# Kernel tuning notes

Hardware: AMD Instinct MI355X
Metric: run time of the kernel (lower is better)

## Reference

```python
import jax, jax.numpy as jnp
import numpy as np

D_MODEL = 4096
D_LATENT = 512
NUM_HEADS = 32
HEAD_DIM = D_MODEL // NUM_HEADS  # 128
ROPE_THETA = 10000.0
BATCH, SEQ = 2, 2048


def _rotate_half(x):
    x1, x2 = jnp.split(x, 2, axis=-1)
    return jnp.concatenate([-x2, x1], axis=-1)


def _rope_cos_sin(positions, head_dim, theta, dtype):
    # positions: [B, S] -> cos/sin: [B, S, 1, head_dim]
    inv_freq = 1.0 / (theta ** (jnp.arange(0, head_dim, 2, dtype=jnp.float32) / head_dim))
    freqs = positions.astype(jnp.float32)[..., None] * inv_freq  # [B,S,hd/2]
    emb = jnp.concatenate([freqs, freqs], axis=-1)               # [B,S,hd]
    return jnp.cos(emb)[:, :, None, :].astype(dtype), jnp.sin(emb)[:, :, None, :].astype(dtype)


def setup_inputs() -> dict:
    key = jax.random.key(0)
    ks = jax.random.split(key, 6)
    s = 0.02
    return {
        "hidden_states": jax.random.normal(ks[0], (BATCH, SEQ, D_MODEL), jnp.float32),
        "Wq": jax.random.normal(ks[1], (D_MODEL, NUM_HEADS * HEAD_DIM), jnp.float32) * s,
        "Wc": jax.random.normal(ks[2], (D_MODEL, D_LATENT), jnp.float32) * s,
        "Wk": jax.random.normal(ks[3], (D_LATENT, NUM_HEADS * HEAD_DIM), jnp.float32) * s,
        "Wv": jax.random.normal(ks[4], (D_LATENT, NUM_HEADS * HEAD_DIM), jnp.float32) * s,
        "Wo": jax.random.normal(ks[5], (NUM_HEADS * HEAD_DIM, D_MODEL), jnp.float32) * s,
    }


def reference(hidden_states, Wq, Wc, Wk, Wv, Wo):
    B, S, _ = hidden_states.shape
    H, Dh = NUM_HEADS, HEAD_DIM

    q = (hidden_states @ Wq).reshape(B, S, H, Dh)
    kv_latent = hidden_states @ Wc                     # [B,S,d_latent]
    k = (kv_latent @ Wk).reshape(B, S, H, Dh)
    v = (kv_latent @ Wv).reshape(B, S, H, Dh)

    # RoPE: q uses positions [0..S), k uses positions [0..S) (no past cache)
    pos = jnp.broadcast_to(jnp.arange(S)[None, :], (B, S))
    cos, sin = _rope_cos_sin(pos, Dh, ROPE_THETA, q.dtype)
    q = q * cos + _rotate_half(q) * sin
    k = k * cos + _rotate_half(k) * sin

    # standard attention, no mask (faithful to attention_mask=None path)
    scale = 1.0 / np.sqrt(Dh)
    scores = jnp.einsum("bqhd,bkhd->bhqk", q, k) * scale
    probs = jax.nn.softmax(scores, axis=-1)
    attn = jnp.einsum("bhqk,bkhd->bqhd", probs, v)     # [B,S,H,Dh]

    out = attn.reshape(B, S, H * Dh) @ Wo
    return out
```

## Files before the change

### kernel.cpp

```cpp
#include <hip/hip_runtime.h>
#include <hip/hip_bf16.h>
#include <cstdint>
#include <cstddef>

#define D_MODEL 4096
#define D_LATENT 512
#define NUM_HEADS 32
#define HEAD_DIM 128
#define BATCH 2
#define SEQ 2048
#define ROWS (BATCH*SEQ)

typedef __attribute__((ext_vector_type(8))) short bf16x8;
typedef __attribute__((ext_vector_type(4))) float f32x4;
typedef __attribute__((ext_vector_type(16))) float f32x16;
typedef unsigned int uint;

static __device__ __forceinline__ unsigned short f2bf(float f){
  union { float f; uint32_t u; } v; v.f = f;
  uint32_t r = (v.u + 0x7fffu + ((v.u >> 16) & 1u)) >> 16;
  return (unsigned short)r;
}
static __device__ __forceinline__ float bf2f(unsigned short h){
  union { uint32_t u; float f; } v; v.u = ((uint32_t)h) << 16;
  return v.f;
}
static __device__ __forceinline__ uint cvtpk(float lo, float hi2){
  uint r;
  asm("v_cvt_pk_bf16_f32 %0, %1, %2" : "=v"(r) : "v"(lo), "v"(hi2));
  return r;
}
static __device__ __forceinline__ void gload16(const void* g, void* l){
  __builtin_amdgcn_global_load_lds(
      (const __attribute__((address_space(1))) void*)g,
      (__attribute__((address_space(3))) void*)l, 16, 0, 0);
}

__global__ __launch_bounds__(256) void f32_to_bf16(
    const float* __restrict__ in, unsigned short* __restrict__ out){
  const size_t i = ((size_t)blockIdx.x * 256 + threadIdx.x) * 8;
  const float4 lo = *(const float4*)(in + i);
  const float4 hi = *(const float4*)(in + i + 4);
  uint4 d; unsigned short* dp = (unsigned short*)&d;
  dp[0]=f2bf(lo.x); dp[1]=f2bf(lo.y); dp[2]=f2bf(lo.z); dp[3]=f2bf(lo.w);
  dp[4]=f2bf(hi.x); dp[5]=f2bf(hi.y); dp[6]=f2bf(hi.z); dp[7]=f2bf(hi.w);
  *(uint4*)(out + i) = d;
}

__global__ __launch_bounds__(256) void transpose_convert(
    const float* __restrict__ W, unsigned short* __restrict__ Wt, int K, int N){
  __shared__ float tile[64][65];
  const int k0 = blockIdx.x * 64, n0 = blockIdx.y * 64;
  const int t = threadIdx.x;
  #pragma unroll
  for (int j = 0; j < 16; ++j){
    const int idx = t + 256*j;
    const int r = idx >> 6, c = idx & 63;
    tile[r][c] = W[(size_t)(k0 + r) * N + n0 + c];
  }
  __syncthreads();
  #pragma unroll
  for (int j = 0; j < 16; ++j){
    const int idx = t + 256*j;
    const int r = idx >> 6, c = idx & 63;
    Wt[(size_t)(n0 + r) * K + k0 + c] = f2bf(tile[c][r]);
  }
}

__global__ __launch_bounds__(256) void v_transpose(
    const unsigned short* __restrict__ v, unsigned short* __restrict__ vt){
  __shared__ unsigned short tile[64][72];
  const int s0 = blockIdx.x * 64, d0 = blockIdx.y * 64, bh = blockIdx.z;
  const int b = bh >> 5, h = bh & 31;
  const int t = threadIdx.x;
  #pragma unroll
  for (int j = 0; j < 2; ++j){
    const int idx = t + 256*j;
    const int r = idx >> 3, ch = idx & 7;
    *(uint4*)&tile[r][ch*8] =
      *(const uint4*)&v[(size_t)(b*SEQ + s0 + r) * D_MODEL + h*128 + d0 + ch*8];
  }
  __syncthreads();
  #pragma unroll
  for (int j = 0; j < 16; ++j){
    const int idx = t + 256*j;
    const int r = idx >> 6, c = idx & 63;
    vt[((size_t)bh*128 + d0 + r) * SEQ + s0 + c] = tile[c][r];
  }
}

__global__ __launch_bounds__(256) void rope_table_kernel(float* __restrict__ ct,
                                                         float* __restrict__ st){
  const int i = blockIdx.x * 256 + threadIdx.x;
  if (i >= SEQ * 64) return;
  const int s = i >> 6, j = i & 63;
  const float inv = powf(10000.0f, -(float)j / 64.0f);
  const double a = (double)s * (double)inv;
  ct[i] = (float)cos(a);
  st[i] = (float)sin(a);
}

__global__ __launch_bounds__(256) void rope_apply(unsigned short* __restrict__ buf,
    const float* __restrict__ ct, const float* __restrict__ st, float scale){
  const int i = blockIdx.x * 256 + threadIdx.x;
  const int j = i & 63;
  const int tmp = i >> 6;
  const int h = tmp & 31;
  const int row = tmp >> 5;
  const int s = row & (SEQ - 1);
  const float c = ct[s*64 + j], sn = st[s*64 + j];
  const size_t base = (size_t)row * D_MODEL + (size_t)h * 128;
  const float x1 = bf2f(buf[base + j]);
  const float x2 = bf2f(buf[base + j + 64]);
  buf[base + j]      = f2bf((x1 * c - x2 * sn) * scale);
  buf[base + j + 64] = f2bf((x2 * c + x1 * sn) * scale);
}

template<bool OF32>
__global__ __launch_bounds__(256) void gemm_kernel(
    const unsigned short* __restrict__ A, const unsigned short* __restrict__ Bt,
    void* __restrict__ Cp, int M, int N, int K){
  __shared__ __align__(16) char As[128 * 128];
  __shared__ __align__(16) char Bs[128 * 128];
  const int t = threadIdx.x;
  const int m0 = blockIdx.y * 128, n0 = blockIdx.x * 128;
  const int l = t & 63, wid = t >> 6;
  const int wr = wid >> 1, wcn = wid & 1;
  const int lr = l & 15, lg = l >> 4;

  const int srow = l >> 3;
  const int gch  = (l & 7) ^ srow;
  const unsigned short* gA = A  + (size_t)(m0 + wid*32 + srow) * K + gch*8;
  const unsigned short* gB = Bt + (size_t)(n0 + wid*32 + srow) * K + gch*8;
  char* lA = As + wid*4096;
  char* lB = Bs + wid*4096;

  f32x4 acc[4][4];
  #pragma unroll
  for (int i = 0; i < 4; ++i)
    #pragma unroll
    for (int j = 0; j < 4; ++j)
      #pragma unroll
      for (int r = 0; r < 4; ++r) acc[i][j][r] = 0.0f;

  const int kTiles = K >> 6;
  for (int kt = 0; kt < kTiles; ++kt){
    const size_t ko = (size_t)kt << 6;
    #pragma unroll
    for (int i = 0; i < 4; ++i){
      gload16(gA + (size_t)i*8*K + ko, lA + i*1024);
      gload16(gB + (size_t)i*8*K + ko, lB + i*1024);
    }
    __syncthreads();
    #pragma unroll
    for (int kc = 0; kc < 2; ++kc){
      bf16x8 af[4], bfv[4];
      const int ch = kc*4 + lg;
      #pragma unroll
      for (int mb = 0; mb < 4; ++mb){
        const int row = wr*64 + mb*16 + lr;
        af[mb] = *(const bf16x8*)(As + row*128 + ((ch ^ (row & 7)) * 16));
      }
      #pragma unroll
      for (int nb = 0; nb < 4; ++nb){
        const int row = wcn*64 + nb*16 + lr;
        bfv[nb] = *(const bf16x8*)(Bs + row*128 + ((ch ^ (row & 7)) * 16));
      }
      #pragma unroll
      for (int mb = 0; mb < 4; ++mb)
        #pragma unroll
        for (int nb = 0; nb < 4; ++nb)
          acc[mb][nb] = __builtin_amdgcn_mfma_f32_16x16x32_bf16(af[mb], bfv[nb], acc[mb][nb], 0, 0, 0);
    }
    __syncthreads();
  }
  #pragma unroll
  for (int mb = 0; mb < 4; ++mb)
    #pragma unroll
    for (int nb = 0; nb < 4; ++nb)
      #pragma unroll
      for (int r = 0; r < 4; ++r){
        const int row = m0 + wr*64 + mb*16 + lg*4 + r;
        const int col = n0 + wcn*64 + nb*16 + lr;
        if constexpr (OF32) ((float*)Cp)[(size_t)row * N + col] = acc[mb][nb][r];
        else ((unsigned short*)Cp)[(size_t)row * N + col] = f2bf(acc[mb][nb][r]);
      }
}

template<int MH>
static __device__ __forceinline__ void rdAh(bf16x8 (&a_)[4][2], const char* buf,
                                            int wr, int lr, int lg){
  #pragma unroll
  for (int mm = 0; mm < 4; ++mm)
    #pragma unroll
    for (int kc = 0; kc < 2; ++kc){
      const int row = wr*128 + (MH*4 + mm)*16 + lr;
      const int ch = kc*4 + lg;
      a_[mm][kc] = *(const bf16x8*)(buf + row*128 + ((ch ^ (row & 7)) * 16));
    }
}
template<int NH>
static __device__ __forceinline__ void rdBh(bf16x8 (&b_)[2][2][2], const char* buf,
                                            int wc, int lr, int lg){
  #pragma unroll
  for (int nn = 0; nn < 2; ++nn)
    #pragma unroll
    for (int kc = 0; kc < 2; ++kc){
      const int row = wc*64 + (NH*2 + nn)*16 + lr;
      const int ch = kc*4 + lg;
      b_[NH][nn][kc] = *(const bf16x8*)(buf + row*128 + ((ch ^ (row & 7)) * 16));
    }
}
template<int MH, int NH>
static __device__ __forceinline__ void mfq(f32x4 (&acc)[8][4],
    const bf16x8 (&a_)[4][2], const bf16x8 (&b_)[2][2][2]){
  __builtin_amdgcn_s_setprio(1);
  #pragma unroll
  for (int kc = 0; kc < 2; ++kc)
    #pragma unroll
    for (int mm = 0; mm < 4; ++mm)
      #pragma unroll
      for (int nn = 0; nn < 2; ++nn)
        acc[MH*4+mm][NH*2+nn] = __builtin_amdgcn_mfma_f32_16x16x32_bf16(
            a_[mm][kc], b_[NH][nn][kc], acc[MH*4+mm][NH*2+nn], 0, 0, 0);
  __builtin_amdgcn_s_setprio(0);
}

#define G256_BAR  __builtin_amdgcn_s_barrier()
#define G256_LGK0 do{ asm volatile("s_waitcnt lgkmcnt(0)" ::: "memory"); \
                      __builtin_amdgcn_sched_barrier(0); }while(0)
#define G256_VM(n) asm volatile("s_waitcnt vmcnt(" #n ")" ::: "memory")

template<bool OF32>
__global__ __launch_bounds__(512, 2) void gemm256_kernel(
    const unsigned short* __restrict__ A, const unsigned short* __restrict__ Bt,
    void* __restrict__ Cp, void* __restrict__ Cp2, int nsplit, int ldc,
    int M, int N, int K){
  __shared__ __align__(16) char lds[131072];
  char* const As0 = lds;
  char* const As1 = lds + 32768;
  char* const Bs0 = lds + 65536;
  char* const Bs1 = lds + 98304;

  const int t = threadIdx.x;
  const int l = t & 63, wid = t >> 6;
  const int wr = wid >> 2, wc = wid & 3;
  const int lr = l & 15, lg = l >> 4;
  const int m0 = blockIdx.y * 256, n0 = blockIdx.x * 256;

  const int srow = t >> 3;
  const int pch = t & 7;
  const int gch = pch ^ (srow & 7);
  const unsigned short* gAb = A  + (size_t)(m0 + srow) * K + gch*8;
  const unsigned short* gBb = Bt + (size_t)(n0 + srow) * K + gch*8;
  const int ldso = srow*128 + pch*16;

  auto stA = [&](char* dst, int half, int kcol){
    const unsigned short* g = gAb + (size_t)half*128*K + kcol;
    gload16(g,                dst + half*16384 + ldso);
    gload16(g + (size_t)64*K, dst + half*16384 + 8192 + ldso);
  };
  auto stB = [&](char* dst, int half, int kcol){
    const unsigned short* g = gBb + (size_t)half*128*K + kcol;
    gload16(g,                dst + half*16384 + ldso);
    gload16(g + (size_t)64*K, dst + half*16384 + 8192 + ldso);
  };

  f32x4 acc[8][4];
  #pragma unroll
  for (int m = 0; m < 8; ++m)
    #pragma unroll
    for (int n = 0; n < 4; ++n)
      #pragma unroll
      for (int r = 0; r < 4; ++r) acc[m][n][r] = 0.0f;
  bf16x8 a_[4][2];
  bf16x8 b_[2][2][2];

  const int niter = K >> 7;
  stA(As0, 0, 0); stA(As0, 1, 0); stB(Bs0, 0, 0); stB(Bs0, 1, 0);
  stA(As1, 0, 64);
  G256_VM(2);
  G256_BAR;
  __builtin_amdgcn_sched_barrier(0);

  for (int j = 0; j < niter; ++j){
    const int k0 = j << 7;
    const bool more = (j + 1 < niter);
    rdAh<0>(a_, As0, wr, lr, lg);
    rdBh<0>(b_, Bs0, wc, lr, lg);
    stA(As1, 1, k0 + 64);
    G256_BAR; G256_LGK0;
    mfq<0,0>(acc, a_, b_);
    G256_BAR;
    rdBh<1>(b_, Bs0, wc, lr, lg);
    stB(Bs1, 0, k0 + 64);
    G256_BAR; G256_LGK0;
    mfq<0,1>(acc, a_, b_);
    G256_BAR;
    rdAh<1>(a_, As0, wr, lr, lg);
    stB(Bs1, 1, k0 + 64);
    G256_BAR; G256_LGK0;
    mfq<1,0>(acc, a_, b_);
    G256_BAR;
    if (more){ stA(As0, 0, k0 + 128); G256_VM(2); }
    else     { G256_VM(0); }
    G256_BAR;
    __builtin_amdgcn_sched_barrier(0);
    mfq<1,1>(acc, a_, b_);
    G256_BAR;
    rdAh<0>(a_, As1, wr, lr, lg);
    rdBh<0>(b_, Bs1, wc, lr, lg);
    if (more) stA(As0, 1, k0 + 128);
    G256_BAR; G256_LGK0;
    mfq<0,0>(acc, a_, b_);
    G256_BAR;
    rdBh<1>(b_, Bs1, wc, lr, lg);
    if (more) stB(Bs0, 0, k0 + 128);
    G256_BAR; G256_LGK0;
    mfq<0,1>(acc, a_, b_);
    G256_BAR;
    rdAh<1>(a_, As1, wr, lr, lg);
    if (more) stB(Bs0, 1, k0 + 128);
    G256_BAR; G256_LGK0;
    mfq<1,0>(acc, a_, b_);
    G256_BAR;
    if (more){ stA(As1, 0, k0 + 192); G256_VM(2); }
    G256_BAR;
    __builtin_amdgcn_sched_barrier(0);
    mfq<1,1>(acc, a_, b_);
    G256_BAR;
  }

  void* outp = Cp;
  int c0 = n0;
  if (n0 >= nsplit){ outp = Cp2; c0 = n0 - nsplit; }
  #pragma unroll
  for (int m = 0; m < 8; ++m)
    #pragma unroll
    for (int n = 0; n < 4; ++n)
      #pragma unroll
      for (int r = 0; r < 4; ++r){
        const int row = m0 + wr*128 + m*16 + lg*4 + r;
        const int col = c0 + wc*64 + n*16 + lr;
        if constexpr (OF32) ((float*)outp)[(size_t)row * ldc + col] = acc[m][n][r];
        else ((unsigned short*)outp)[(size_t)row * ldc + col] = f2bf(acc[m][n][r]);
      }
}

__global__ __launch_bounds__(512) void attn_kernel(
    const unsigned short* __restrict__ q, const unsigned short* __restrict__ kp,
    const unsigned short* __restrict__ vt, const float* __restrict__ ct,
    const float* __restrict__ st, unsigned short* __restrict__ o){
  __shared__ __align__(16) char Ks[2 * 16384];
  __shared__ __align__(16) char Vs[2 * 16384];
  const int t = threadIdx.x;
  const int l = t & 63, w = t >> 6;
  const int lq = l & 31, hi = l >> 5;
  const int bh = blockIdx.x, qb = blockIdx.y;
  const int b = bh >> 5;
  const size_t qbase = (size_t)b * SEQ + qb*256 + w*32;
  const size_t cb = (size_t)(bh & 31) * 128;

  auto stageK = [&](int buf, int kb){
    const size_t kr0 = (size_t)b * SEQ + (size_t)kb*64;
    char* kdst = Ks + buf*16384 + w*2048;
    #pragma unroll
    for (int i = 0; i < 2; ++i){
      const int r = w*8 + i*4 + (l >> 4);
      const int g = (l & 15) ^ (r & 15);
      gload16(kp + (kr0 + r) * D_MODEL + cb + g*8, kdst + i*1024);
    }
  };
  auto stageV = [&](int buf, int kb){
    char* vdst = Vs + buf*16384 + w*2048;
    #pragma unroll
    for (int i = 0; i < 2; ++i){
      const int r = w*16 + i*8 + (l >> 3);
      const int g = (l & 7) ^ (r & 7);
      gload16(vt + ((size_t)bh*128 + r) * SEQ + (size_t)kb*64 + g*8, vdst + i*1024);
    }
  };

  bf16x8 qf[8];
  #pragma unroll
  for (int dc = 0; dc < 8; ++dc)
    qf[dc] = *(const bf16x8*)(q + (qbase + lq) * D_MODEL + cb + dc*16 + hi*8);
  {
    const float qsc = 0.08838834764831845f * 1.4426950408889634f;
    const int s = qb*256 + w*32 + lq;
    #pragma unroll
    for (int dc = 0; dc < 4; ++dc){
      const int j0 = dc*16 + hi*8;
      const float4 c0 = *(const float4*)(ct + s*64 + j0);
      const float4 c1 = *(const float4*)(ct + s*64 + j0 + 4);
      const float4 s0_ = *(const float4*)(st + s*64 + j0);
      const float4 s1_ = *(const float4*)(st + s*64 + j0 + 4);
      const float cc[8] = {c0.x,c0.y,c0.z,c0.w,c1.x,c1.y,c1.z,c1.w};
      const float ss[8] = {s0_.x,s0_.y,s0_.z,s0_.w,s1_.x,s1_.y,s1_.z,s1_.w};
      #pragma unroll
      for (int e = 0; e < 8; ++e){
        const float x1 = bf2f((unsigned short)qf[dc][e]);
        const float x2 = bf2f((unsigned short)qf[dc + 4][e]);
        qf[dc][e]     = (short)f2bf((x1 * cc[e] - x2 * ss[e]) * qsc);
        qf[dc + 4][e] = (short)f2bf((x2 * cc[e] + x1 * ss[e]) * qsc);
      }
    }
  }

  f32x16 O[4];
  #pragma unroll
  for (int nb = 0; nb < 4; ++nb)
    #pragma unroll
    for (int r = 0; r < 16; ++r) O[nb][r] = 0.0f;
  float m = -1e30f, lsum = 0.0f;

  stageK(0, 0); stageV(0, 0);

  for (int kb = 0; kb < SEQ/64; ++kb){
    const bool more = (kb + 1 < SEQ/64);
    asm volatile("s_waitcnt vmcnt(0)" ::: "memory");
    __builtin_amdgcn_s_barrier();
    __builtin_amdgcn_sched_barrier(0);
    if (more){ stageK((kb + 1) & 1, kb + 1); stageV((kb + 1) & 1, kb + 1); }
    const char* Kb = Ks + (kb & 1)*16384;
    const char* Vb = Vs + (kb & 1)*16384;

    f32x16 s0, s1;
    #pragma unroll
    for (int r = 0; r < 16; ++r){ s0[r] = 0.0f; s1[r] = 0.0f; }
    __builtin_amdgcn_s_setprio(1);
    #pragma unroll
    for (int dc = 0; dc < 8; ++dc){
      const int ch = dc*2 + hi;
      const bf16x8 k0 = *(const bf16x8*)(Kb + lq*256 + ((ch ^ (lq & 15)) * 16));
      const bf16x8 k1 = *(const bf16x8*)(Kb + (32 + lq)*256 + ((ch ^ (lq & 15)) * 16));
      s0 = __builtin_amdgcn_mfma_f32_32x32x16_bf16(k0, qf[dc], s0, 0, 0, 0);
      s1 = __builtin_amdgcn_mfma_f32_32x32x16_bf16(k1, qf[dc], s1, 0, 0, 0);
    }
    __builtin_amdgcn_s_setprio(0);

    float mt = s0[0];
    #pragma unroll
    for (int r = 1; r < 16; ++r) mt = fmaxf(mt, s0[r]);
    #pragma unroll
    for (int r = 0; r < 16; ++r) mt = fmaxf(mt, s1[r]);
    mt = fmaxf(mt, __shfl_xor(mt, 32));

    if (!__all(mt <= m + 8.0f)){
      const float mnew = fmaxf(m, mt);
      const float al = __builtin_amdgcn_exp2f(m - mnew);
      m = mnew;
      lsum *= al;
      #pragma unroll
      for (int r = 0; r < 16; ++r){
        const int crow = (r & 3) + 8*(r >> 2) + 4*hi;
        const float albr = __shfl(al, crow);
        #pragma unroll
        for (int nb = 0; nb < 4; ++nb) O[nb][r] *= albr;
      }
    }

    float E[32];
    float sum = 0.0f;
    #pragma unroll
    for (int r = 0; r < 16; ++r){ E[r] = __builtin_amdgcn_exp2f(s0[r] - m); sum += E[r]; }
    #pragma unroll
    for (int r = 0; r < 16; ++r){ E[16 + r] = __builtin_amdgcn_exp2f(s1[r] - m); sum += E[16 + r]; }
    sum += __shfl_xor(sum, 32);
    lsum += sum;

    bf16x8 pa[4];
    #pragma unroll
    for (int c = 0; c < 4; ++c){
      const int rb = c * 8;
      const uint a_ = cvtpk(E[rb + 0], E[rb + 1]);
      const uint b_ = cvtpk(E[rb + 2], E[rb + 3]);
      const uint c_ = cvtpk(E[rb + 4], E[rb + 5]);
      const uint d_ = cvtpk(E[rb + 6], E[rb + 7]);
      const uint sa = (uint)__shfl_xor((int)a_, 32);
      const uint sb = (uint)__shfl_xor((int)b_, 32);
      const uint sc = (uint)__shfl_xor((int)c_, 32);
      const uint sd = (uint)__shfl_xor((int)d_, 32);
      union { uint u[4]; bf16x8 v; } uu;
      uu.u[0] = hi ? sc : a_;
      uu.u[1] = hi ? sd : b_;
      uu.u[2] = hi ? c_ : sa;
      uu.u[3] = hi ? d_ : sb;
      pa[c] = uu.v;
    }

    __builtin_amdgcn_s_setprio(1);
    #pragma unroll
    for (int c = 0; c < 4; ++c){
      const int ch = c*2 + hi;
      #pragma unroll
      for (int nb = 0; nb < 4; ++nb){
        const int vr = nb*32 + lq;
        const bf16x8 vf = *(const bf16x8*)(Vb + vr*128 + ((ch ^ (vr & 7)) * 16));
        O[nb] = __builtin_amdgcn_mfma_f32_32x32x16_bf16(pa[c], vf, O[nb], 0, 0, 0);
      }
    }
    __builtin_amdgcn_s_setprio(0);
  }

  const float rinv = 1.0f / lsum;
  #pragma unroll
  for (int r = 0; r < 16; ++r){
    const int crow = (r & 3) + 8*(r >> 2) + 4*hi;
    const float rb_ = __shfl(rinv, crow);
    #pragma unroll
    for (int nb = 0; nb < 4; ++nb)
      o[(qbase + crow) * D_MODEL + cb + nb*32 + lq] = f2bf(O[nb][r] * rb_);
  }
}

extern "C" void kernel_launch(void* const* d_in, const int* in_sizes, int n_in,
                              void* d_out, int out_size, void* d_ws, size_t ws_size,
                              hipStream_t stream){
  const float* hidden = (const float*)d_in[0];
  const float* Wq = (const float*)d_in[1];
  const float* Wc = (const float*)d_in[2];
  const float* Wk = (const float*)d_in[3];
  const float* Wv = (const float*)d_in[4];
  const float* Wo = (const float*)d_in[5];
  float* out = (float*)d_out;

  char* ws = (char*)d_ws;
  size_t off = 0;
  auto alloc = [&](size_t bytes)->char*{
    char* p = ws + off; off += (bytes + 255) & ~(size_t)255; return p;
  };
  unsigned short* Wqt  = (unsigned short*)alloc((size_t)D_MODEL * D_MODEL * 2);
  unsigned short* Wct  = (unsigned short*)alloc((size_t)D_LATENT * D_MODEL * 2);
  unsigned short* Wkvt = (unsigned short*)alloc((size_t)2 * D_MODEL * D_LATENT * 2);
  unsigned short* Wot  = (unsigned short*)alloc((size_t)D_MODEL * D_MODEL * 2);
  unsigned short* latent = (unsigned short*)alloc((size_t)ROWS * D_LATENT * 2);
  unsigned short* qbuf = (unsigned short*)alloc((size_t)ROWS * D_MODEL * 2);
  unsigned short* kbuf = (unsigned short*)alloc((size_t)ROWS * D_MODEL * 2);
  unsigned short* vbuf = (unsigned short*)alloc((size_t)ROWS * D_MODEL * 2);
  unsigned short* attnb= (unsigned short*)alloc((size_t)ROWS * D_MODEL * 2);
  float* ctab = (float*)alloc((size_t)SEQ * 64 * 4);
  float* stab = (float*)alloc((size_t)SEQ * 64 * 4);
  unsigned short* hbf   = attnb;
  unsigned short* vtbuf = Wqt;

  const dim3 B256(256);

  f32_to_bf16<<<(ROWS*(size_t)D_MODEL)/2048, B256, 0, stream>>>(hidden, hbf);
  transpose_convert<<<dim3(64, 64), B256, 0, stream>>>(Wq, Wqt, D_MODEL, D_MODEL);
  transpose_convert<<<dim3(64, 8),  B256, 0, stream>>>(Wc, Wct, D_MODEL, D_LATENT);
  transpose_convert<<<dim3(8, 64),  B256, 0, stream>>>(Wk, Wkvt, D_LATENT, D_MODEL);
  transpose_convert<<<dim3(8, 64),  B256, 0, stream>>>(Wv, Wkvt + (size_t)D_MODEL*D_LATENT, D_LATENT, D_MODEL);
  transpose_convert<<<dim3(64, 64), B256, 0, stream>>>(Wo, Wot, D_MODEL, D_MODEL);
  rope_table_kernel<<<512, B256, 0, stream>>>(ctab, stab);

  gemm_kernel<false><<<dim3(D_LATENT/128, ROWS/128), B256, 0, stream>>>(hbf, Wct, latent, ROWS, D_LATENT, D_MODEL);
  gemm256_kernel<false><<<dim3(D_MODEL/256, ROWS/256), dim3(512), 0, stream>>>(
      hbf, Wqt, qbuf, qbuf, 1 << 30, D_MODEL, ROWS, D_MODEL, D_MODEL);
  gemm256_kernel<false><<<dim3(2*D_MODEL/256, ROWS/256), dim3(512), 0, stream>>>(
      latent, Wkvt, kbuf, vbuf, D_MODEL, D_MODEL, ROWS, 2*D_MODEL, D_LATENT);

  v_transpose<<<dim3(SEQ/64, HEAD_DIM/64, BATCH*NUM_HEADS), B256, 0, stream>>>(vbuf, vtbuf);

  rope_apply<<<(ROWS * NUM_HEADS * 64) / 256, B256, 0, stream>>>(kbuf, ctab, stab, 1.0f);

  attn_kernel<<<dim3(BATCH * NUM_HEADS, SEQ/256), dim3(512), 0, stream>>>(
      qbuf, kbuf, vtbuf, ctab, stab, attnb);

  gemm256_kernel<true><<<dim3(D_MODEL/256, ROWS/256), dim3(512), 0, stream>>>(
      attnb, Wot, out, out, 1 << 30, D_MODEL, ROWS, D_MODEL, D_MODEL);
}
```

Baseline: 642.4 us.

## Fuse V transpose into KV GEMM epilogue and tree-reduce softmax max/sum

```diff
diff --git a/kernel.cpp b/kernel.cpp
--- a/kernel.cpp
+++ b/kernel.cpp
@@ -64,28 +64,6 @@
     const int idx = t + 256*j;
     const int r = idx >> 6, c = idx & 63;
     Wt[(size_t)(n0 + r) * K + k0 + c] = f2bf(tile[c][r]);
-  }
-}
-
-__global__ __launch_bounds__(256) void v_transpose(
-    const unsigned short* __restrict__ v, unsigned short* __restrict__ vt){
-  __shared__ unsigned short tile[64][72];
-  const int s0 = blockIdx.x * 64, d0 = blockIdx.y * 64, bh = blockIdx.z;
-  const int b = bh >> 5, h = bh & 31;
-  const int t = threadIdx.x;
-  #pragma unroll
-  for (int j = 0; j < 2; ++j){
-    const int idx = t + 256*j;
-    const int r = idx >> 3, ch = idx & 7;
-    *(uint4*)&tile[r][ch*8] =
-      *(const uint4*)&v[(size_t)(b*SEQ + s0 + r) * D_MODEL + h*128 + d0 + ch*8];
-  }
-  __syncthreads();
-  #pragma unroll
-  for (int j = 0; j < 16; ++j){
-    const int idx = t + 256*j;
-    const int r = idx >> 6, c = idx & 63;
-    vt[((size_t)bh*128 + d0 + r) * SEQ + s0 + c] = tile[c][r];
   }
 }
 
@@ -235,7 +213,7 @@
 __global__ __launch_bounds__(512, 2) void gemm256_kernel(
     const unsigned short* __restrict__ A, const unsigned short* __restrict__ Bt,
     void* __restrict__ Cp, void* __restrict__ Cp2, int nsplit, int ldc,
-    int M, int N, int K){
+    int M, int N, int K, int vt_mode){
   __shared__ __align__(16) char lds[131072];
   char* const As0 = lds;
   char* const As1 = lds + 32768;
@@ -331,6 +309,22 @@
     G256_BAR;
   }
 
+  if (n0 >= nsplit && vt_mode){
+    unsigned short* vtp = (unsigned short*)Cp2;
+    #pragma unroll
+    for (int m = 0; m < 8; ++m)
+      #pragma unroll
+      for (int n = 0; n < 4; ++n)
+        #pragma unroll
+        for (int r = 0; r < 4; ++r){
+          const int row = m0 + wr*128 + m*16 + lg*4 + r;
+          const int col = (n0 - nsplit) + wc*64 + n*16 + lr;
+          const size_t didx = ((size_t)(((row >> 11) << 5) | (col >> 7)) * 128
+                               + (col & 127)) * SEQ + (row & (SEQ - 1));
+          vtp[didx] = f2bf(acc[m][n][r]);
+        }
+    return;
+  }
   void* outp = Cp;
   int c0 = n0;
   if (n0 >= nsplit){ outp = Cp2; c0 = n0 - nsplit; }
@@ -439,11 +433,13 @@
     }
     __builtin_amdgcn_s_setprio(0);
 
-    float mt = s0[0];
-    #pragma unroll
-    for (int r = 1; r < 16; ++r) mt = fmaxf(mt, s0[r]);
-    #pragma unroll
-    for (int r = 0; r < 16; ++r) mt = fmaxf(mt, s1[r]);
+    float tm[8];
+    #pragma unroll
+    for (int r = 0; r < 8; ++r)
+      tm[r] = fmaxf(fmaxf(s0[r], s0[r + 8]), fmaxf(s1[r], s1[r + 8]));
+    #pragma unroll
+    for (int r = 0; r < 4; ++r) tm[r] = fmaxf(tm[r], tm[r + 4]);
+    float mt = fmaxf(fmaxf(tm[0], tm[1]), fmaxf(tm[2], tm[3]));
     mt = fmaxf(mt, __shfl_xor(mt, 32));
 
     if (!__all(mt <= m + 8.0f)){
@@ -461,11 +457,17 @@
     }
 
     float E[32];
-    float sum = 0.0f;
-    #pragma unroll
-    for (int r = 0; r < 16; ++r){ E[r] = __builtin_amdgcn_exp2f(s0[r] - m); sum += E[r]; }
-    #pragma unroll
-    for (int r = 0; r < 16; ++r){ E[16 + r] = __builtin_amdgcn_exp2f(s1[r] - m); sum += E[16 + r]; }
+    #pragma unroll
+    for (int r = 0; r < 16; ++r) E[r] = __builtin_amdgcn_exp2f(s0[r] - m);
+    #pragma unroll
+    for (int r = 0; r < 16; ++r) E[16 + r] = __builtin_amdgcn_exp2f(s1[r] - m);
+    float ts[8];
+    #pragma unroll
+    for (int r = 0; r < 8; ++r)
+      ts[r] = (E[r] + E[r + 8]) + (E[r + 16] + E[r + 24]);
+    #pragma unroll
+    for (int r = 0; r < 4; ++r) ts[r] += ts[r + 4];
+    float sum = (ts[0] + ts[1]) + (ts[2] + ts[3]);
     sum += __shfl_xor(sum, 32);
     lsum += sum;
 
@@ -477,15 +479,15 @@
       const uint b_ = cvtpk(E[rb + 2], E[rb + 3]);
       const uint c_ = cvtpk(E[rb + 4], E[rb + 5]);
       const uint d_ = cvtpk(E[rb + 6], E[rb + 7]);
-      const uint sa = (uint)__shfl_xor((int)a_, 32);
-      const uint sb = (uint)__shfl_xor((int)b_, 32);
-      const uint sc = (uint)__shfl_xor((int)c_, 32);
-      const uint sd = (uint)__shfl_xor((int)d_, 32);
+      const uint x = hi ? a_ : c_;
+      const uint y = hi ? b_ : d_;
+      const uint sx = (uint)__shfl_xor((int)x, 32);
+      const uint sy = (uint)__shfl_xor((int)y, 32);
       union { uint u[4]; bf16x8 v; } uu;
-      uu.u[0] = hi ? sc : a_;
-      uu.u[1] = hi ? sd : b_;
-      uu.u[2] = hi ? c_ : sa;
-      uu.u[3] = hi ? d_ : sb;
+      uu.u[0] = hi ? sx : a_;
+      uu.u[1] = hi ? sy : b_;
+      uu.u[2] = hi ? c_ : sx;
+      uu.u[3] = hi ? d_ : sy;
       pa[c] = uu.v;
     }
 
@@ -556,11 +558,9 @@
 
   gemm_kernel<false><<<dim3(D_LATENT/128, ROWS/128), B256, 0, stream>>>(hbf, Wct, latent, ROWS, D_LATENT, D_MODEL);
   gemm256_kernel<false><<<dim3(D_MODEL/256, ROWS/256), dim3(512), 0, stream>>>(
-      hbf, Wqt, qbuf, qbuf, 1 << 30, D_MODEL, ROWS, D_MODEL, D_MODEL);
+      hbf, Wqt, qbuf, qbuf, 1 << 30, D_MODEL, ROWS, D_MODEL, D_MODEL, 0);
   gemm256_kernel<false><<<dim3(2*D_MODEL/256, ROWS/256), dim3(512), 0, stream>>>(
-      latent, Wkvt, kbuf, vbuf, D_MODEL, D_MODEL, ROWS, 2*D_MODEL, D_LATENT);
-
-  v_transpose<<<dim3(SEQ/64, HEAD_DIM/64, BATCH*NUM_HEADS), B256, 0, stream>>>(vbuf, vtbuf);
+      latent, Wkvt, kbuf, vtbuf, D_MODEL, D_MODEL, ROWS, 2*D_MODEL, D_LATENT, 1);
 
   rope_apply<<<(ROWS * NUM_HEADS * 64) / 256, B256, 0, stream>>>(kbuf, ctab, stab, 1.0f);
 
@@ -568,5 +568,5 @@
       qbuf, kbuf, vtbuf, ctab, stab, attnb);
 
   gemm256_kernel<true><<<dim3(D_MODEL/256, ROWS/256), dim3(512), 0, stream>>>(
-      attnb, Wot, out, out, 1 << 30, D_MODEL, ROWS, D_MODEL, D_MODEL);
-}
+      attnb, Wot, out, out, 1 << 30, D_MODEL, ROWS, D_MODEL, D_MODEL, 0);
+}
```

Result: no change. 631.8 us (-1.7%).

## Merge latent and Q projections; write transposed V from KV GEMM epilogue

Applied to the files above, without the earlier changes.

```diff
diff --git a/kernel.cpp b/kernel.cpp
--- a/kernel.cpp
+++ b/kernel.cpp
@@ -64,28 +64,6 @@
     const int idx = t + 256*j;
     const int r = idx >> 6, c = idx & 63;
     Wt[(size_t)(n0 + r) * K + k0 + c] = f2bf(tile[c][r]);
-  }
-}
-
-__global__ __launch_bounds__(256) void v_transpose(
-    const unsigned short* __restrict__ v, unsigned short* __restrict__ vt){
-  __shared__ unsigned short tile[64][72];
-  const int s0 = blockIdx.x * 64, d0 = blockIdx.y * 64, bh = blockIdx.z;
-  const int b = bh >> 5, h = bh & 31;
-  const int t = threadIdx.x;
-  #pragma unroll
-  for (int j = 0; j < 2; ++j){
-    const int idx = t + 256*j;
-    const int r = idx >> 3, ch = idx & 7;
-    *(uint4*)&tile[r][ch*8] =
-      *(const uint4*)&v[(size_t)(b*SEQ + s0 + r) * D_MODEL + h*128 + d0 + ch*8];
-  }
-  __syncthreads();
-  #pragma unroll
-  for (int j = 0; j < 16; ++j){
-    const int idx = t + 256*j;
-    const int r = idx >> 6, c = idx & 63;
-    vt[((size_t)bh*128 + d0 + r) * SEQ + s0 + c] = tile[c][r];
   }
 }
 
@@ -116,77 +94,6 @@
   buf[base + j + 64] = f2bf((x2 * c + x1 * sn) * scale);
 }
 
-template<bool OF32>
-__global__ __launch_bounds__(256) void gemm_kernel(
-    const unsigned short* __restrict__ A, const unsigned short* __restrict__ Bt,
-    void* __restrict__ Cp, int M, int N, int K){
-  __shared__ __align__(16) char As[128 * 128];
-  __shared__ __align__(16) char Bs[128 * 128];
-  const int t = threadIdx.x;
-  const int m0 = blockIdx.y * 128, n0 = blockIdx.x * 128;
-  const int l = t & 63, wid = t >> 6;
-  const int wr = wid >> 1, wcn = wid & 1;
-  const int lr = l & 15, lg = l >> 4;
-
-  const int srow = l >> 3;
-  const int gch  = (l & 7) ^ srow;
-  const unsigned short* gA = A  + (size_t)(m0 + wid*32 + srow) * K + gch*8;
-  const unsigned short* gB = Bt + (size_t)(n0 + wid*32 + srow) * K + gch*8;
-  char* lA = As + wid*4096;
-  char* lB = Bs + wid*4096;
-
-  f32x4 acc[4][4];
-  #pragma unroll
-  for (int i = 0; i < 4; ++i)
-    #pragma unroll
-    for (int j = 0; j < 4; ++j)
-      #pragma unroll
-      for (int r = 0; r < 4; ++r) acc[i][j][r] = 0.0f;
-
-  const int kTiles = K >> 6;
-  for (int kt = 0; kt < kTiles; ++kt){
-    const size_t ko = (size_t)kt << 6;
-    #pragma unroll
-    for (int i = 0; i < 4; ++i){
-      gload16(gA + (size_t)i*8*K + ko, lA + i*1024);
-      gload16(gB + (size_t)i*8*K + ko, lB + i*1024);
-    }
-    __syncthreads();
-    #pragma unroll
-    for (int kc = 0; kc < 2; ++kc){
-      bf16x8 af[4], bfv[4];
-      const int ch = kc*4 + lg;
-      #pragma unroll
-      for (int mb = 0; mb < 4; ++mb){
-        const int row = wr*64 + mb*16 + lr;
-        af[mb] = *(const bf16x8*)(As + row*128 + ((ch ^ (row & 7)) * 16));
-      }
-      #pragma unroll
-      for (int nb = 0; nb < 4; ++nb){
-        const int row = wcn*64 + nb*16 + lr;
-        bfv[nb] = *(const bf16x8*)(Bs + row*128 + ((ch ^ (row & 7)) * 16));
-      }
-      #pragma unroll
-      for (int mb = 0; mb < 4; ++mb)
-        #pragma unroll
-        for (int nb = 0; nb < 4; ++nb)
-          acc[mb][nb] = __builtin_amdgcn_mfma_f32_16x16x32_bf16(af[mb], bfv[nb], acc[mb][nb], 0, 0, 0);
-    }
-    __syncthreads();
-  }
-  #pragma unroll
-  for (int mb = 0; mb < 4; ++mb)
-    #pragma unroll
-    for (int nb = 0; nb < 4; ++nb)
-      #pragma unroll
-      for (int r = 0; r < 4; ++r){
-        const int row = m0 + wr*64 + mb*16 + lg*4 + r;
-        const int col = n0 + wcn*64 + nb*16 + lr;
-        if constexpr (OF32) ((float*)Cp)[(size_t)row * N + col] = acc[mb][nb][r];
-        else ((unsigned short*)Cp)[(size_t)row * N + col] = f2bf(acc[mb][nb][r]);
-      }
-}
-
 template<int MH>
 static __device__ __forceinline__ void rdAh(bf16x8 (&a_)[4][2], const char* buf,
                                             int wr, int lr, int lg){
@@ -234,8 +141,8 @@
 template<bool OF32>
 __global__ __launch_bounds__(512, 2) void gemm256_kernel(
     const unsigned short* __restrict__ A, const unsigned short* __restrict__ Bt,
-    void* __restrict__ Cp, void* __restrict__ Cp2, int nsplit, int ldc,
-    int M, int N, int K){
+    void* __restrict__ Cp, void* __restrict__ Cp2, int nsplit, int ldc, int ldc2,
+    int M, int N, int K, int vt_mode){
   __shared__ __align__(16) char lds[131072];
   char* const As0 = lds;
   char* const As1 = lds + 32768;
@@ -331,9 +238,25 @@
     G256_BAR;
   }
 
+  if (n0 >= nsplit && vt_mode){
+    unsigned short* vtp = (unsigned short*)Cp2;
+    #pragma unroll
+    for (int m = 0; m < 8; ++m)
+      #pragma unroll
+      for (int n = 0; n < 4; ++n)
+        #pragma unroll
+        for (int r = 0; r < 4; ++r){
+          const int row = m0 + wr*128 + m*16 + lg*4 + r;
+          const int col = (n0 - nsplit) + wc*64 + n*16 + lr;
+          const size_t didx = ((size_t)(((row >> 11) << 5) | (col >> 7)) * 128
+                               + (col & 127)) * SEQ + (row & (SEQ - 1));
+          vtp[didx] = f2bf(acc[m][n][r]);
+        }
+    return;
+  }
   void* outp = Cp;
-  int c0 = n0;
-  if (n0 >= nsplit){ outp = Cp2; c0 = n0 - nsplit; }
+  int c0 = n0, ld = ldc;
+  if (n0 >= nsplit){ outp = Cp2; c0 = n0 - nsplit; ld = ldc2; }
   #pragma unroll
   for (int m = 0; m < 8; ++m)
     #pragma unroll
@@ -342,8 +265,8 @@
       for (int r = 0; r < 4; ++r){
         const int row = m0 + wr*128 + m*16 + lg*4 + r;
         const int col = c0 + wc*64 + n*16 + lr;
-        if constexpr (OF32) ((float*)outp)[(size_t)row * ldc + col] = acc[m][n][r];
-        else ((unsigned short*)outp)[(size_t)row * ldc + col] = f2bf(acc[m][n][r]);
+        if constexpr (OF32) ((float*)outp)[(size_t)row * ld + col] = acc[m][n][r];
+        else ((unsigned short*)outp)[(size_t)row * ld + col] = f2bf(acc[m][n][r]);
       }
 }
 
@@ -530,37 +453,32 @@
   auto alloc = [&](size_t bytes)->char*{
     char* p = ws + off; off += (bytes + 255) & ~(size_t)255; return p;
   };
-  unsigned short* Wqt  = (unsigned short*)alloc((size_t)D_MODEL * D_MODEL * 2);
-  unsigned short* Wct  = (unsigned short*)alloc((size_t)D_LATENT * D_MODEL * 2);
+  unsigned short* Wqct = (unsigned short*)alloc((size_t)(D_MODEL + D_LATENT) * D_MODEL * 2);
   unsigned short* Wkvt = (unsigned short*)alloc((size_t)2 * D_MODEL * D_LATENT * 2);
   unsigned short* Wot  = (unsigned short*)alloc((size_t)D_MODEL * D_MODEL * 2);
   unsigned short* latent = (unsigned short*)alloc((size_t)ROWS * D_LATENT * 2);
   unsigned short* qbuf = (unsigned short*)alloc((size_t)ROWS * D_MODEL * 2);
   unsigned short* kbuf = (unsigned short*)alloc((size_t)ROWS * D_MODEL * 2);
-  unsigned short* vbuf = (unsigned short*)alloc((size_t)ROWS * D_MODEL * 2);
   unsigned short* attnb= (unsigned short*)alloc((size_t)ROWS * D_MODEL * 2);
   float* ctab = (float*)alloc((size_t)SEQ * 64 * 4);
   float* stab = (float*)alloc((size_t)SEQ * 64 * 4);
   unsigned short* hbf   = attnb;
-  unsigned short* vtbuf = Wqt;
+  unsigned short* vtbuf = Wqct;
 
   const dim3 B256(256);
 
   f32_to_bf16<<<(ROWS*(size_t)D_MODEL)/2048, B256, 0, stream>>>(hidden, hbf);
-  transpose_convert<<<dim3(64, 64), B256, 0, stream>>>(Wq, Wqt, D_MODEL, D_MODEL);
-  transpose_convert<<<dim3(64, 8),  B256, 0, stream>>>(Wc, Wct, D_MODEL, D_LATENT);
+  transpose_convert<<<dim3(64, 64), B256, 0, stream>>>(Wq, Wqct, D_MODEL, D_MODEL);
+  transpose_convert<<<dim3(64, 8),  B256, 0, stream>>>(Wc, Wqct + (size_t)D_MODEL*D_MODEL, D_MODEL, D_LATENT);
   transpose_convert<<<dim3(8, 64),  B256, 0, stream>>>(Wk, Wkvt, D_LATENT, D_MODEL);
   transpose_convert<<<dim3(8, 64),  B256, 0, stream>>>(Wv, Wkvt + (size_t)D_MODEL*D_LATENT, D_LATENT, D_MODEL);
   transpose_convert<<<dim3(64, 64), B256, 0, stream>>>(Wo, Wot, D_MODEL, D_MODEL);
   rope_table_kernel<<<512, B256, 0, stream>>>(ctab, stab);
 
-  gemm_kernel<false><<<dim3(D_LATENT/128, ROWS/128), B256, 0, stream>>>(hbf, Wct, latent, ROWS, D_LATENT, D_MODEL);
-  gemm256_kernel<false><<<dim3(D_MODEL/256, ROWS/256), dim3(512), 0, stream>>>(
-      hbf, Wqt, qbuf, qbuf, 1 << 30, D_MODEL, ROWS, D_MODEL, D_MODEL);
+  gemm256_kernel<false><<<dim3((D_MODEL + D_LATENT)/256, ROWS/256), dim3(512), 0, stream>>>(
+      hbf, Wqct, qbuf, latent, D_MODEL, D_MODEL, D_LATENT, ROWS, D_MODEL + D_LATENT, D_MODEL, 0);
   gemm256_kernel<false><<<dim3(2*D_MODEL/256, ROWS/256), dim3(512), 0, stream>>>(
-      latent, Wkvt, kbuf, vbuf, D_MODEL, D_MODEL, ROWS, 2*D_MODEL, D_LATENT);
-
-  v_transpose<<<dim3(SEQ/64, HEAD_DIM/64, BATCH*NUM_HEADS), B256, 0, stream>>>(vbuf, vtbuf);
+      latent, Wkvt, kbuf, vtbuf, D_MODEL, D_MODEL, 0, ROWS, 2*D_MODEL, D_LATENT, 1);
 
   rope_apply<<<(ROWS * NUM_HEADS * 64) / 256, B256, 0, stream>>>(kbuf, ctab, stab, 1.0f);
 
@@ -568,5 +486,5 @@
       qbuf, kbuf, vtbuf, ctab, stab, attnb);
 
   gemm256_kernel<true><<<dim3(D_MODEL/256, ROWS/256), dim3(512), 0, stream>>>(
-      attnb, Wot, out, out, 1 << 30, D_MODEL, ROWS, D_MODEL, D_MODEL);
-}
+      attnb, Wot, out, out, 1 << 30, D_MODEL, D_MODEL, ROWS, D_MODEL, D_MODEL, 0);
+}
```

Result: no change. 642.9 us (+0.1%).

## Fuse V transpose into KV GEMM epilogue and remap blocks per XCD

Applied to the files above, without the earlier changes.

```diff
diff --git a/kernel.cpp b/kernel.cpp
--- a/kernel.cpp
+++ b/kernel.cpp
@@ -64,28 +64,6 @@
     const int idx = t + 256*j;
     const int r = idx >> 6, c = idx & 63;
     Wt[(size_t)(n0 + r) * K + k0 + c] = f2bf(tile[c][r]);
-  }
-}
-
-__global__ __launch_bounds__(256) void v_transpose(
-    const unsigned short* __restrict__ v, unsigned short* __restrict__ vt){
-  __shared__ unsigned short tile[64][72];
-  const int s0 = blockIdx.x * 64, d0 = blockIdx.y * 64, bh = blockIdx.z;
-  const int b = bh >> 5, h = bh & 31;
-  const int t = threadIdx.x;
-  #pragma unroll
-  for (int j = 0; j < 2; ++j){
-    const int idx = t + 256*j;
-    const int r = idx >> 3, ch = idx & 7;
-    *(uint4*)&tile[r][ch*8] =
-      *(const uint4*)&v[(size_t)(b*SEQ + s0 + r) * D_MODEL + h*128 + d0 + ch*8];
-  }
-  __syncthreads();
-  #pragma unroll
-  for (int j = 0; j < 16; ++j){
-    const int idx = t + 256*j;
-    const int r = idx >> 6, c = idx & 63;
-    vt[((size_t)bh*128 + d0 + r) * SEQ + s0 + c] = tile[c][r];
   }
 }
 
@@ -123,7 +101,11 @@
   __shared__ __align__(16) char As[128 * 128];
   __shared__ __align__(16) char Bs[128 * 128];
   const int t = threadIdx.x;
-  const int m0 = blockIdx.y * 128, n0 = blockIdx.x * 128;
+  const int nbx = gridDim.x;
+  const int nwg = nbx * gridDim.y;
+  int bid = blockIdx.y * nbx + blockIdx.x;
+  bid = (bid & 7) * (nwg >> 3) + (bid >> 3);
+  const int m0 = (bid / nbx) * 128, n0 = (bid % nbx) * 128;
   const int l = t & 63, wid = t >> 6;
   const int wr = wid >> 1, wcn = wid & 1;
   const int lr = l & 15, lg = l >> 4;
@@ -234,8 +216,8 @@
 template<bool OF32>
 __global__ __launch_bounds__(512, 2) void gemm256_kernel(
     const unsigned short* __restrict__ A, const unsigned short* __restrict__ Bt,
-    void* __restrict__ Cp, void* __restrict__ Cp2, int nsplit, int ldc,
-    int M, int N, int K){
+    void* __restrict__ Cp, void* __restrict__ Cp2, int nsplit, int ldc, int ldc2,
+    int M, int N, int K, int vt_mode){
   __shared__ __align__(16) char lds[131072];
   char* const As0 = lds;
   char* const As1 = lds + 32768;
@@ -246,7 +228,11 @@
   const int l = t & 63, wid = t >> 6;
   const int wr = wid >> 2, wc = wid & 3;
   const int lr = l & 15, lg = l >> 4;
-  const int m0 = blockIdx.y * 256, n0 = blockIdx.x * 256;
+  const int nbx = gridDim.x;
+  const int nwg = nbx * gridDim.y;
+  int bid = blockIdx.y * nbx + blockIdx.x;
+  bid = (bid & 7) * (nwg >> 3) + (bid >> 3);
+  const int m0 = (bid / nbx) * 256, n0 = (bid % nbx) * 256;
 
   const int srow = t >> 3;
   const int pch = t & 7;
@@ -331,9 +317,25 @@
     G256_BAR;
   }
 
+  if (n0 >= nsplit && vt_mode){
+    unsigned short* vtp = (unsigned short*)Cp2;
+    #pragma unroll
+    for (int m = 0; m < 8; ++m)
+      #pragma unroll
+      for (int n = 0; n < 4; ++n)
+        #pragma unroll
+        for (int r = 0; r < 4; ++r){
+          const int row = m0 + wr*128 + m*16 + lg*4 + r;
+          const int col = (n0 - nsplit) + wc*64 + n*16 + lr;
+          const size_t didx = ((size_t)(((row >> 11) << 5) | (col >> 7)) * 128
+                               + (col & 127)) * SEQ + (row & (SEQ - 1));
+          vtp[didx] = f2bf(acc[m][n][r]);
+        }
+    return;
+  }
   void* outp = Cp;
-  int c0 = n0;
-  if (n0 >= nsplit){ outp = Cp2; c0 = n0 - nsplit; }
+  int c0 = n0, ld = ldc;
+  if (n0 >= nsplit){ outp = Cp2; c0 = n0 - nsplit; ld = ldc2; }
   #pragma unroll
   for (int m = 0; m < 8; ++m)
     #pragma unroll
@@ -342,8 +344,8 @@
       for (int r = 0; r < 4; ++r){
         const int row = m0 + wr*128 + m*16 + lg*4 + r;
         const int col = c0 + wc*64 + n*16 + lr;
-        if constexpr (OF32) ((float*)outp)[(size_t)row * ldc + col] = acc[m][n][r];
-        else ((unsigned short*)outp)[(size_t)row * ldc + col] = f2bf(acc[m][n][r]);
+        if constexpr (OF32) ((float*)outp)[(size_t)row * ld + col] = acc[m][n][r];
+        else ((unsigned short*)outp)[(size_t)row * ld + col] = f2bf(acc[m][n][r]);
       }
 }
 
@@ -537,7 +539,6 @@
   unsigned short* latent = (unsigned short*)alloc((size_t)ROWS * D_LATENT * 2);
   unsigned short* qbuf = (unsigned short*)alloc((size_t)ROWS * D_MODEL * 2);
   unsigned short* kbuf = (unsigned short*)alloc((size_t)ROWS * D_MODEL * 2);
-  unsigned short* vbuf = (unsigned short*)alloc((size_t)ROWS * D_MODEL * 2);
   unsigned short* attnb= (unsigned short*)alloc((size_t)ROWS * D_MODEL * 2);
   float* ctab = (float*)alloc((size_t)SEQ * 64 * 4);
   float* stab = (float*)alloc((size_t)SEQ * 64 * 4);
@@ -554,13 +555,12 @@
   transpose_convert<<<dim3(64, 64), B256, 0, stream>>>(Wo, Wot, D_MODEL, D_MODEL);
   rope_table_kernel<<<512, B256, 0, stream>>>(ctab, stab);
 
-  gemm_kernel<false><<<dim3(D_LATENT/128, ROWS/128), B256, 0, stream>>>(hbf, Wct, latent, ROWS, D_LATENT, D_MODEL);
+  gemm_kernel<false><<<dim3(D_LATENT/128, ROWS/128), B256, 0, stream>>>(
+      hbf, Wct, latent, ROWS, D_LATENT, D_MODEL);
   gemm256_kernel<false><<<dim3(D_MODEL/256, ROWS/256), dim3(512), 0, stream>>>(
-      hbf, Wqt, qbuf, qbuf, 1 << 30, D_MODEL, ROWS, D_MODEL, D_MODEL);
+      hbf, Wqt, qbuf, qbuf, 1 << 30, D_MODEL, D_MODEL, ROWS, D_MODEL, D_MODEL, 0);
   gemm256_kernel<false><<<dim3(2*D_MODEL/256, ROWS/256), dim3(512), 0, stream>>>(
-      latent, Wkvt, kbuf, vbuf, D_MODEL, D_MODEL, ROWS, 2*D_MODEL, D_LATENT);
-
-  v_transpose<<<dim3(SEQ/64, HEAD_DIM/64, BATCH*NUM_HEADS), B256, 0, stream>>>(vbuf, vtbuf);
+      latent, Wkvt, kbuf, vtbuf, D_MODEL, D_MODEL, 0, ROWS, 2*D_MODEL, D_LATENT, 1);
 
   rope_apply<<<(ROWS * NUM_HEADS * 64) / 256, B256, 0, stream>>>(kbuf, ctab, stab, 1.0f);
 
@@ -568,5 +568,5 @@
       qbuf, kbuf, vtbuf, ctab, stab, attnb);
 
   gemm256_kernel<true><<<dim3(D_MODEL/256, ROWS/256), dim3(512), 0, stream>>>(
-      attnb, Wot, out, out, 1 << 30, D_MODEL, ROWS, D_MODEL, D_MODEL);
-}
+      attnb, Wot, out, out, 1 << 30, D_MODEL, D_MODEL, ROWS, D_MODEL, D_MODEL, 0);
+}
```

New measurement: 609.6 us. 1.05x faster.
